# Optimization experiments

Hardware: AMD Instinct MI355X
Metric: run time of the kernel (lower is better)

Reference implementation:

```python
import jax, jax.numpy as jnp
import numpy as np

N, F, H, C, HX, E = 50000, 256, 128, 16, 64, 500000
TEMP = 1.0


def gcn_conv(x, src, dst, W, b, n):
    # PyG GCNConv: x @ W, add self-loops, sym-normalized scatter-sum src->dst
    xw = x @ W
    idx = jnp.arange(n)
    s = jnp.concatenate([src, idx])
    d = jnp.concatenate([dst, idx])
    deg = jax.ops.segment_sum(jnp.ones_like(s, dtype=xw.dtype), d, num_segments=n)
    dinv = jnp.where(deg > 0, jax.lax.rsqrt(deg), 0.0)
    norm = dinv[s] * dinv[d]
    out = jax.ops.segment_sum(xw[s] * norm[:, None], d, num_segments=n)
    return out + b


def setup_inputs() -> dict:
    key = jax.random.key(0)
    ks = jax.random.split(key, 16)
    x = jax.random.normal(ks[0], (N, F), jnp.float32)
    edge_index = jax.random.randint(ks[1], (2, E), 0, N)
    neg_edge_index = jax.random.randint(ks[2], (2, E), 0, N)
    y = jax.random.randint(ks[3], (N,), 0, C)
    train_mask = jax.random.uniform(ks[4], (N,)) < 0.5
    def lin(k, fi, fo):
        s = 1.0 / np.sqrt(fi)
        return jax.random.uniform(k, (fi, fo), jnp.float32, -s, s)
    W1 = lin(ks[5], F, H); b1 = jnp.zeros((H,), jnp.float32)
    W2 = lin(ks[6], H, C); b2 = jnp.zeros((C,), jnp.float32)
    Wx = lin(ks[7], F, HX); bx = jnp.zeros((HX,), jnp.float32)
    Wd = lin(ks[8], 2 * (HX + C), 1); bd = jnp.zeros((1,), jnp.float32)
    return dict(x=x, edge_index=edge_index, neg_edge_index=neg_edge_index, y=y,
                train_mask=train_mask, W1=W1, b1=b1, W2=W2, b2=b2,
                Wx=Wx, bx=bx, Wd=Wd, bd=bd)


def reference(x, edge_index, neg_edge_index, y, train_mask,
              W1, b1, W2, b2, Wx, bx, Wd, bd):
    n = x.shape[0]
    # GNN encoder p(y|x,G): 2-layer GCN (eval mode -> dropout identity)
    h = jax.nn.relu(gcn_conv(x, edge_index[0], edge_index[1], W1, b1, n))
    logits = gcn_conv(h, edge_index[0], edge_index[1], W2, b2, n) / TEMP
    y_log_prob = jax.nn.log_softmax(logits, axis=-1)
    y_prob = jnp.where(train_mask[:, None],
                       jax.nn.one_hot(y, logits.shape[-1], dtype=logits.dtype),
                       jnp.exp(y_log_prob))
    # node feature encoder
    xe = jax.nn.relu(x @ Wx + bx)
    def decode(ei):
        s, d = ei[0], ei[1]
        feat = jnp.concatenate([xe[s], xe[d], y_prob[s], y_prob[d]], axis=1)
        return feat @ Wd + bd
    e_pred_pos = decode(edge_index)
    e_pred_neg = decode(neg_edge_index)
    return e_pred_pos, e_pred_neg, y_log_prob
```

## Files before the change

### kernel.cpp

```cpp
#include <hip/hip_runtime.h>
#include <hip/hip_fp16.h>

typedef unsigned short ushort_t;
typedef __attribute__((ext_vector_type(8))) short short8;
typedef __attribute__((ext_vector_type(4))) float floatx4;

constexpr int F = 256, H = 128, C = 16, HX = 64;
constexpr int NBCOL = H + HX;
constexpr int MAXS = 64;

__device__ __forceinline__ ushort_t f2bf(float f) {
  unsigned u = __float_as_uint(f);
  u += 0x7fffu + ((u >> 16) & 1u);
  return (ushort_t)(u >> 16);
}

__global__ void k_pre(const float* __restrict__ x, ushort_t* __restrict__ xb, int totalU,
                      const float* __restrict__ W1, const float* __restrict__ Wx,
                      ushort_t* __restrict__ WBt,
                      const int* __restrict__ src, const int* __restrict__ dst,
                      int* __restrict__ cursor, int2* __restrict__ csr8, int e,
                      int n, int nbe, int nbx) {
  int b = blockIdx.x;
  if (b < nbe) {
    int t = b * 256 + threadIdx.x;
    int i0 = 2 * t;
    if (i0 >= e) return;
    if (i0 + 1 < e) {
      int2 s2 = ((const int2*)src)[t];
      int2 d2 = ((const int2*)dst)[t];
      int p0 = atomicAdd(&cursor[d2.x], 1);
      int p1 = atomicAdd(&cursor[d2.y], 1);
      ((int*)csr8)[2 * (d2.x * MAXS + p0)] = s2.x;
      ((int*)csr8)[2 * (d2.y * MAXS + p1)] = s2.y;
    } else {
      int s = src[i0], d = dst[i0];
      int p = atomicAdd(&cursor[d], 1);
      ((int*)csr8)[2 * (d * MAXS + p)] = s;
    }
  } else if (b < nbe + nbx) {
    int i = (b - nbe) * 256 + threadIdx.x;
    if (i >= totalU) return;
    int tile = i >> 9, rem = i & 511, j = rem >> 4, l15 = rem & 15;
    int row = tile * 16 + l15;
    ushort4 lo = make_ushort4(0, 0, 0, 0), hi = lo;
    if (row < n) {
      const float4* xp = (const float4*)(x + (size_t)row * F + j * 8);
      float4 a = xp[0], bb = xp[1];
      lo = make_ushort4(f2bf(a.x), f2bf(a.y), f2bf(a.z), f2bf(a.w));
      hi = make_ushort4(f2bf(bb.x), f2bf(bb.y), f2bf(bb.z), f2bf(bb.w));
    }
    ((ushort4*)xb)[2 * i] = lo;
    ((ushort4*)xb)[2 * i + 1] = hi;
  } else {
    int i = (b - nbe - nbx) * 256 + threadIdx.x;
    if (i >= NBCOL * F) return;
    int nn = i / F, k = i % F;
    float v = (nn < H) ? W1[k * H + nn] : Wx[k * HX + (nn - H)];
    WBt[nn * F + k] = f2bf(v);
  }
}

__global__ void k_pad(const int* __restrict__ cursor, int2* __restrict__ csr8, int n) {
  int i = blockIdx.x * 256 + threadIdx.x;
  int v = i >> 6, t = i & 63;
  if (v >= n) return;
  int base = v * MAXS;
  int deg = cursor[v];
  int cur = base + deg;
  int pe = base + ((deg + 16) & ~15);
  int p = base + t;
  if (p < cur) {
    int s = ((const int*)csr8)[2 * p];
    float w = rsqrtf((float)(cursor[s] + 1));
    csr8[p] = make_int2(s, __float_as_int(w));
  } else if (p < pe) {
    float w = (p == cur) ? rsqrtf((float)(deg + 1)) : 0.0f;
    csr8[p] = make_int2(v, __float_as_int(w));
  }
}

__global__ __launch_bounds__(256, 3) void k_gemm1(const ushort_t* __restrict__ xb,
                                                  const ushort_t* __restrict__ WBt,
                                                  const float* __restrict__ bx,
                                                  ushort_t* __restrict__ xw1,
                                                  float* __restrict__ xe,
                                                  int n, int ntiles) {
  int w = threadIdx.x >> 6, lane = threadIdx.x & 63;
  int q = lane >> 4, l15 = lane & 15;
  const short8* bb = (const short8*)WBt;
  short8 bfr[3][8];
#pragma unroll
  for (int t = 0; t < 3; t++)
#pragma unroll
    for (int kk = 0; kk < 8; kk++)
      bfr[t][kk] = bb[(size_t)(w * 48 + t * 16 + l15) * 32 + kk * 4 + q];

  float bxv[3];
#pragma unroll
  for (int t = 0; t < 3; t++) {
    int g = w * 48 + t * 16;
    bxv[t] = (g >= H) ? bx[g - H + l15] : 0.0f;
  }

  const short8* ab = (const short8*)xb;
  for (int tile = blockIdx.x; tile < ntiles; tile += gridDim.x) {
    const short8* atile = ab + (size_t)tile * 512;
    short8 a[8];
#pragma unroll
    for (int kk = 0; kk < 8; kk++) a[kk] = atile[kk * 64 + q * 16 + l15];

    floatx4 acc0 = (floatx4)(0.0f), acc1 = (floatx4)(0.0f), acc2 = (floatx4)(0.0f);
#pragma unroll
    for (int kk = 0; kk < 8; kk++) {
      acc0 = __builtin_amdgcn_mfma_f32_16x16x32_bf16(a[kk], bfr[0][kk], acc0, 0, 0, 0);
      acc1 = __builtin_amdgcn_mfma_f32_16x16x32_bf16(a[kk], bfr[1][kk], acc1, 0, 0, 0);
      acc2 = __builtin_amdgcn_mfma_f32_16x16x32_bf16(a[kk], bfr[2][kk], acc2, 0, 0, 0);
    }

    floatx4 accs[3] = {acc0, acc1, acc2};
    int rbase = tile * 16 + q * 4;
#pragma unroll
    for (int t = 0; t < 3; t++) {
      int g = w * 48 + t * 16;
#pragma unroll
      for (int r = 0; r < 4; r++) {
        int ro = rbase + r;
        if (ro < n) {
          if (g < H) {
            __half hv = __float2half(accs[t][r]);
            xw1[(size_t)ro * H + g + l15] = *reinterpret_cast<ushort_t*>(&hv);
          } else {
            xe[(size_t)ro * HX + (g - H) + l15] = fmaxf(accs[t][r] + bxv[t], 0.0f);
          }
        }
      }
    }
  }
}

__global__ __launch_bounds__(256, 4) void k_agg1g2(const ushort_t* __restrict__ xw1,
                         const int* __restrict__ cursor,
                         const int2* __restrict__ csr8,
                         const float* __restrict__ b1, const float* __restrict__ W2,
                         float* __restrict__ hw2, int n) {
  __shared__ float hsm[4][128];
  int wid = threadIdx.x >> 6, lane = threadIdx.x & 63;
  int g = lane >> 5, li = lane & 31;
  int c = lane & 15, gg = lane >> 4;
  int c4 = li * 4;

  float w2r[32];
#pragma unroll
  for (int jj = 0; jj < 32; jj++) w2r[jj] = W2[(gg * 32 + jj) * C + c];
  float4 b4 = *(const float4*)(b1 + c4);

  int gwave = blockIdx.x * 4 + wid;
  int nwaves = gridDim.x * 4;
  for (int v = gwave; v < n; v += nwaves) {
    int j0 = v * MAXS;
    int deg = cursor[v];
    int j1 = j0 + ((deg + 16) & ~15);
    float dv = rsqrtf((float)(deg + 1));
    float ax0 = 0.0f, ay0 = 0.0f, ax1 = 0.0f, ay1 = 0.0f;
    for (int j = j0; j < j1; j += 16) {
      int2 ee[8];
      uint2 rr[8];
#pragma unroll
      for (int u = 0; u < 8; u++) ee[u] = csr8[j + g * 8 + u];
#pragma unroll
      for (int u = 0; u < 8; u++)
        rr[u] = ((const uint2*)(xw1 + (size_t)ee[u].x * H))[li];
#pragma unroll
      for (int u = 0; u < 8; u++) {
        float wu = __int_as_float(ee[u].y);
        __half2 p0 = *reinterpret_cast<__half2*>(&rr[u].x);
        __half2 p1 = *reinterpret_cast<__half2*>(&rr[u].y);
        ax0 = fmaf(wu, __low2float(p0), ax0);
        ay0 = fmaf(wu, __high2float(p0), ay0);
        ax1 = fmaf(wu, __low2float(p1), ax1);
        ay1 = fmaf(wu, __high2float(p1), ay1);
      }
    }
    ax0 += __shfl_xor(ax0, 32); ay0 += __shfl_xor(ay0, 32);
    ax1 += __shfl_xor(ax1, 32); ay1 += __shfl_xor(ay1, 32);
    float o0 = fmaxf(fmaf(dv, ax0, b4.x), 0.0f);
    float o1 = fmaxf(fmaf(dv, ay0, b4.y), 0.0f);
    float o2 = fmaxf(fmaf(dv, ax1, b4.z), 0.0f);
    float o3 = fmaxf(fmaf(dv, ay1, b4.w), 0.0f);
    if (g == 0) *(float4*)&hsm[wid][c4] = make_float4(o0, o1, o2, o3);

    const float* hrow = hsm[wid];
    float p = 0.0f;
#pragma unroll
    for (int jj = 0; jj < 32; jj++)
      p = fmaf(hrow[gg * 32 + jj], w2r[jj], p);
    p += __shfl_xor(p, 16);
    p += __shfl_xor(p, 32);
    if (gg == 0) hw2[(size_t)v * C + c] = p;
  }
}

__global__ void k_agg2ab(const float* __restrict__ hw2, const int* __restrict__ cursor,
                         const int2* __restrict__ csr8,
                         const float* __restrict__ b2, const int* __restrict__ y,
                         const int* __restrict__ tmask, const float* __restrict__ xe,
                         const float* __restrict__ Wd, float* __restrict__ ylp_out,
                         float* __restrict__ Aarr, float* __restrict__ Barr, int n) {
  int t = threadIdx.x;
  int c = t & 15;
  float4 wa = *(const float4*)(Wd + c * 4);
  float4 wb = *(const float4*)(Wd + HX + c * 4);
  float wdA = Wd[2 * HX + c], wdB = Wd[2 * HX + C + c];
  float b2c = b2[c];
  int nodestep = gridDim.x * 16;
  for (int node = blockIdx.x * 16 + (t >> 4); node < n; node += nodestep) {
    int j0 = node * MAXS;
    int deg = cursor[node];
    int j1 = j0 + ((deg + 16) & ~15);
    float dv = rsqrtf((float)(deg + 1));
    float acc = 0.0f;
    for (int j = j0; j < j1; j += 16) {
      int2 ee[16];
      float rr[16];
#pragma unroll
      for (int u = 0; u < 16; u++) ee[u] = csr8[j + u];
#pragma unroll
      for (int u = 0; u < 16; u++) rr[u] = hw2[(size_t)ee[u].x * C + c];
#pragma unroll
      for (int u = 0; u < 16; u++) acc = fmaf(__int_as_float(ee[u].y), rr[u], acc);
    }
    float logit = fmaf(dv, acc, b2c);
    float m = logit;
    for (int o = 8; o > 0; o >>= 1) m = fmaxf(m, __shfl_xor(m, o, 16));
    float e = expf(logit - m);
    float s16 = e;
    for (int o = 8; o > 0; o >>= 1) s16 += __shfl_xor(s16, o, 16);
    float lp = (logit - m) - logf(s16);
    ylp_out[(size_t)node * C + c] = lp;
    float yp = tmask[node] ? ((y[node] == c) ? 1.0f : 0.0f) : (e / s16);

    float4 xv = *(const float4*)(xe + (size_t)node * HX + c * 4);
    float pa = xv.x * wa.x + xv.y * wa.y + xv.z * wa.z + xv.w * wa.w + yp * wdA;
    float pb = xv.x * wb.x + xv.y * wb.y + xv.z * wb.z + xv.w * wb.w + yp * wdB;
    for (int o = 8; o > 0; o >>= 1) {
      pa += __shfl_xor(pa, o, 16);
      pb += __shfl_xor(pb, o, 16);
    }
    if (c == 0) { Aarr[node] = pa; Barr[node] = pb; }
  }
}

__global__ void k_decode(const int* __restrict__ ei, const int* __restrict__ nei,
                         const float* __restrict__ Aarr, const float* __restrict__ Barr,
                         const float* __restrict__ bd, float* __restrict__ out, int e) {
  int i = blockIdx.x * 256 + threadIdx.x;
  if (i >= 2 * e) return;
  float b0 = bd[0];
  if (i < e) {
    int s = ei[i], d = ei[e + i];
    out[i] = Aarr[s] + Barr[d] + b0;
  } else {
    int j = i - e;
    int s = nei[j], d = nei[e + j];
    out[e + j] = Aarr[s] + Barr[d] + b0;
  }
}

extern "C" void kernel_launch(void* const* d_in, const int* in_sizes, int n_in,
                              void* d_out, int out_size, void* d_ws, size_t ws_size,
                              hipStream_t stream) {
  const float* x = (const float*)d_in[0];
  const int* ei = (const int*)d_in[1];
  const int* nei = (const int*)d_in[2];
  const int* y = (const int*)d_in[3];
  const int* tmask = (const int*)d_in[4];
  const float* W1 = (const float*)d_in[5];
  const float* b1 = (const float*)d_in[6];
  const float* W2 = (const float*)d_in[7];
  const float* b2 = (const float*)d_in[8];
  const float* Wx = (const float*)d_in[9];
  const float* bx = (const float*)d_in[10];
  const float* Wd = (const float*)d_in[11];
  const float* bd = (const float*)d_in[12];
  float* out = (float*)d_out;

  int n = in_sizes[3];
  int e = in_sizes[1] / 2;
  int ntiles = (n + 15) / 16;

  char* ws = (char*)d_ws;
  size_t off = 0;
  auto alloc = [&](size_t bytes) -> void* {
    void* p = ws + off;
    off += (bytes + 511) & ~(size_t)511;
    return p;
  };
  ushort_t* xb = (ushort_t*)alloc((size_t)ntiles * 16 * F * 2);
  ushort_t* WBt = (ushort_t*)alloc((size_t)NBCOL * F * 2);
  ushort_t* xw1 = (ushort_t*)alloc((size_t)n * H * 2);
  float* xe = (float*)alloc((size_t)n * HX * 4);
  float* hw2 = (float*)alloc((size_t)n * C * 4);
  int* cursor = (int*)alloc((size_t)n * 4);
  int2* csr8 = (int2*)alloc((size_t)n * MAXS * 8);
  float* Aarr = (float*)alloc((size_t)n * 4);
  float* Barr = (float*)alloc((size_t)n * 4);

  const int* src = ei;
  const int* dst = ei + e;

  hipMemsetAsync(cursor, 0, (size_t)n * 4, stream);

  int totalU = ntiles * 512;
  int nbe = ((e + 1) / 2 + 255) / 256;
  int nbx = (totalU + 255) / 256;
  int nbw = (NBCOL * F + 255) / 256;
  k_pre<<<nbe + nbx + nbw, 256, 0, stream>>>(x, xb, totalU, W1, Wx, WBt,
                                             src, dst, cursor, csr8, e,
                                             n, nbe, nbx);
  k_pad<<<(n * MAXS + 255) / 256, 256, 0, stream>>>(cursor, csr8, n);

  int ggrid = ntiles < 768 ? ntiles : 768;
  k_gemm1<<<ggrid, 256, 0, stream>>>(xb, WBt, bx, xw1, xe, n, ntiles);
  int agrid1 = (n + 3) / 4;
  if (agrid1 > 1024) agrid1 = 1024;
  k_agg1g2<<<agrid1, 256, 0, stream>>>(xw1, cursor, csr8, b1, W2, hw2, n);
  int agrid2 = (n * 16 + 255) / 256;
  if (agrid2 > 1024) agrid2 = 1024;
  k_agg2ab<<<agrid2, 256, 0, stream>>>(hw2, cursor, csr8, b2, y,
                                       tmask, xe, Wd, out + (size_t)2 * e,
                                       Aarr, Barr, n);
  k_decode<<<(2 * e + 255) / 256, 256, 0, stream>>>(ei, nei, Aarr, Barr, bd, out, e);
}
```

Baseline: 227.1 us.

## Split per-node edge cursors into two padded counters to cut atomic contention

Edge bucketing now uses two separate atomic counters per destination node, each on its own 64-byte slot, with alternating edges assigned to either half of the 64-entry CSR row. Each thread handles four edges through int4 loads. The pad kernel is reworked to compact the two halves into one list, compute the degree once and store it in a separate degd array that the aggregation kernels read. This is meant to reduce same-address atomic serialization and false sharing on the cursor array, at the cost of a 32x larger cursor memset and extra work in the compaction pass. Each half holds only 32 slots, so a node whose edges land unevenly could overflow a half even when its total degree fits in 64.

```diff
diff --git a/kernel.cpp b/kernel.cpp
--- a/kernel.cpp
+++ b/kernel.cpp
@@ -24,19 +24,29 @@
   int b = blockIdx.x;
   if (b < nbe) {
     int t = b * 256 + threadIdx.x;
-    int i0 = 2 * t;
+    int i0 = 4 * t;
     if (i0 >= e) return;
-    if (i0 + 1 < e) {
-      int2 s2 = ((const int2*)src)[t];
-      int2 d2 = ((const int2*)dst)[t];
-      int p0 = atomicAdd(&cursor[d2.x], 1);
-      int p1 = atomicAdd(&cursor[d2.y], 1);
-      ((int*)csr8)[2 * (d2.x * MAXS + p0)] = s2.x;
-      ((int*)csr8)[2 * (d2.y * MAXS + p1)] = s2.y;
+    if ((e & 3) == 0) {
+      int4 s4 = ((const int4*)src)[t];
+      int4 d4 = ((const int4*)dst)[t];
+      int p0 = atomicAdd(&cursor[(d4.x << 5)], 1);
+      int p1 = atomicAdd(&cursor[(d4.y << 5) + 16], 1);
+      int p2 = atomicAdd(&cursor[(d4.z << 5)], 1);
+      int p3 = atomicAdd(&cursor[(d4.w << 5) + 16], 1);
+      ((int*)csr8)[2 * ((d4.x << 6) + p0)] = s4.x;
+      ((int*)csr8)[2 * ((d4.y << 6) + 32 + p1)] = s4.y;
+      ((int*)csr8)[2 * ((d4.z << 6) + p2)] = s4.z;
+      ((int*)csr8)[2 * ((d4.w << 6) + 32 + p3)] = s4.w;
     } else {
-      int s = src[i0], d = dst[i0];
-      int p = atomicAdd(&cursor[d], 1);
-      ((int*)csr8)[2 * (d * MAXS + p)] = s;
+      for (int k = 0; k < 4; k++) {
+        int i = i0 + k;
+        if (i < e) {
+          int s = src[i], d = dst[i];
+          int r = k & 1;
+          int p = atomicAdd(&cursor[(d << 5) + (r << 4)], 1);
+          ((int*)csr8)[2 * ((d << 6) + (r << 5) + p)] = s;
+        }
+      }
     }
   } else if (b < nbe + nbx) {
     int i = (b - nbe) * 256 + threadIdx.x;
@@ -61,23 +71,29 @@
   }
 }
 
-__global__ void k_pad(const int* __restrict__ cursor, int2* __restrict__ csr8, int n) {
-  int i = blockIdx.x * 256 + threadIdx.x;
-  int v = i >> 6, t = i & 63;
-  if (v >= n) return;
-  int base = v * MAXS;
-  int deg = cursor[v];
-  int cur = base + deg;
-  int pe = base + ((deg + 16) & ~15);
-  int p = base + t;
-  if (p < cur) {
-    int s = ((const int*)csr8)[2 * p];
-    float w = rsqrtf((float)(cursor[s] + 1));
-    csr8[p] = make_int2(s, __float_as_int(w));
-  } else if (p < pe) {
-    float w = (p == cur) ? rsqrtf((float)(deg + 1)) : 0.0f;
-    csr8[p] = make_int2(v, __float_as_int(w));
-  }
+__global__ void k_pad(const int* __restrict__ cursor, int2* __restrict__ csr8,
+                      int* __restrict__ degd, int n) {
+  int node = blockIdx.x * 4 + (threadIdx.x >> 6);
+  if (node >= n) return;
+  int t = threadIdx.x & 63;
+  int c0 = cursor[node << 5];
+  int c1 = cursor[(node << 5) + 16];
+  int deg = c0 + c1;
+  int base = node << 6;
+  int sval = ((const int*)csr8)[2 * (base + t)];
+  int r = t >> 5, sub = t & 31;
+  bool valid = sub < (r ? c1 : c0);
+  int pos = r ? (c0 + sub) : sub;
+  float w = 0.0f;
+  if (valid)
+    w = rsqrtf((float)(cursor[sval << 5] + cursor[(sval << 5) + 16] + 1));
+  int pe = (deg + 16) & ~15;
+  if (valid) csr8[base + pos] = make_int2(sval, __float_as_int(w));
+  if (t == 0) {
+    csr8[base + deg] = make_int2(node, __float_as_int(rsqrtf((float)(deg + 1))));
+    degd[node] = deg;
+  }
+  if (t > deg && t < pe) csr8[base + t] = make_int2(node, 0);
 }
 
 __global__ __launch_bounds__(256, 3) void k_gemm1(const ushort_t* __restrict__ xb,
@@ -140,7 +156,7 @@
 }
 
 __global__ __launch_bounds__(256, 4) void k_agg1g2(const ushort_t* __restrict__ xw1,
-                         const int* __restrict__ cursor,
+                         const int* __restrict__ degd,
                          const int2* __restrict__ csr8,
                          const float* __restrict__ b1, const float* __restrict__ W2,
                          float* __restrict__ hw2, int n) {
@@ -159,7 +175,7 @@
   int nwaves = gridDim.x * 4;
   for (int v = gwave; v < n; v += nwaves) {
     int j0 = v * MAXS;
-    int deg = cursor[v];
+    int deg = degd[v];
     int j1 = j0 + ((deg + 16) & ~15);
     float dv = rsqrtf((float)(deg + 1));
     float ax0 = 0.0f, ay0 = 0.0f, ax1 = 0.0f, ay1 = 0.0f;
@@ -201,7 +217,7 @@
   }
 }
 
-__global__ void k_agg2ab(const float* __restrict__ hw2, const int* __restrict__ cursor,
+__global__ void k_agg2ab(const float* __restrict__ hw2, const int* __restrict__ degd,
                          const int2* __restrict__ csr8,
                          const float* __restrict__ b2, const int* __restrict__ y,
                          const int* __restrict__ tmask, const float* __restrict__ xe,
@@ -216,7 +232,7 @@
   int nodestep = gridDim.x * 16;
   for (int node = blockIdx.x * 16 + (t >> 4); node < n; node += nodestep) {
     int j0 = node * MAXS;
-    int deg = cursor[node];
+    int deg = degd[node];
     int j1 = j0 + ((deg + 16) & ~15);
     float dv = rsqrtf((float)(deg + 1));
     float acc = 0.0f;
@@ -301,7 +317,8 @@
   ushort_t* xw1 = (ushort_t*)alloc((size_t)n * H * 2);
   float* xe = (float*)alloc((size_t)n * HX * 4);
   float* hw2 = (float*)alloc((size_t)n * C * 4);
-  int* cursor = (int*)alloc((size_t)n * 4);
+  int* cursor = (int*)alloc((size_t)n * 32 * 4);
+  int* degd = (int*)alloc((size_t)n * 4);
   int2* csr8 = (int2*)alloc((size_t)n * MAXS * 8);
   float* Aarr = (float*)alloc((size_t)n * 4);
   float* Barr = (float*)alloc((size_t)n * 4);
@@ -309,25 +326,25 @@
   const int* src = ei;
   const int* dst = ei + e;
 
-  hipMemsetAsync(cursor, 0, (size_t)n * 4, stream);
+  hipMemsetAsync(cursor, 0, (size_t)n * 32 * 4, stream);
 
   int totalU = ntiles * 512;
-  int nbe = ((e + 1) / 2 + 255) / 256;
+  int nbe = ((e + 3) / 4 + 255) / 256;
   int nbx = (totalU + 255) / 256;
   int nbw = (NBCOL * F + 255) / 256;
   k_pre<<<nbe + nbx + nbw, 256, 0, stream>>>(x, xb, totalU, W1, Wx, WBt,
                                              src, dst, cursor, csr8, e,
                                              n, nbe, nbx);
-  k_pad<<<(n * MAXS + 255) / 256, 256, 0, stream>>>(cursor, csr8, n);
+  k_pad<<<(n + 3) / 4, 256, 0, stream>>>(cursor, csr8, degd, n);
 
   int ggrid = ntiles < 768 ? ntiles : 768;
   k_gemm1<<<ggrid, 256, 0, stream>>>(xb, WBt, bx, xw1, xe, n, ntiles);
   int agrid1 = (n + 3) / 4;
   if (agrid1 > 1024) agrid1 = 1024;
-  k_agg1g2<<<agrid1, 256, 0, stream>>>(xw1, cursor, csr8, b1, W2, hw2, n);
+  k_agg1g2<<<agrid1, 256, 0, stream>>>(xw1, degd, csr8, b1, W2, hw2, n);
   int agrid2 = (n * 16 + 255) / 256;
   if (agrid2 > 1024) agrid2 = 1024;
-  k_agg2ab<<<agrid2, 256, 0, stream>>>(hw2, cursor, csr8, b2, y,
+  k_agg2ab<<<agrid2, 256, 0, stream>>>(hw2, degd, csr8, b2, y,
                                        tmask, xe, Wd, out + (size_t)2 * e,
                                        Aarr, Barr, n);
   k_decode<<<(2 * e + 255) / 256, 256, 0, stream>>>(ei, nei, Aarr, Barr, bd, out, e);
```

New measurement: 232.4 us. 1.02x slower.
